# Kernel tuning notes

Measured on AMD Instinct MI355X. Metric: run time of the kernel, lower is better.

Reference implementation:

```python
import jax, jax.numpy as jnp
import numpy as np

B, S, D_IN = 16, 512, 768
HID, OUT = 64, 12
NEG = 1e12


def setup_inputs() -> dict:
    key = jax.random.key(0)
    k1, k2, k3 = jax.random.split(key, 3)
    x = jax.random.normal(k1, (B, S, D_IN), dtype=jnp.float32)
    mask = jnp.ones((B, S), dtype=jnp.float32)
    W = jax.random.normal(k2, (D_IN, HID * OUT * 2), dtype=jnp.float32) * 0.02
    b = jax.random.normal(k3, (HID * OUT * 2,), dtype=jnp.float32) * 0.02
    return {"x": x, "mask": mask, "W": W, "b": b}


def reference(x, mask, W, b):
    Bb, Ss, _ = x.shape
    h, out = HID, OUT
    # QKV-style projection, split into `out` heads of 2h each
    proj = (x @ W + b).reshape(Bb, Ss, out, 2 * h)  # [b, s, out, 2h]
    qw, kw = proj[..., :h], proj[..., h:]           # [b, s, out, h]

    # Sinusoidal position embedding (merge='zero'): interleaved sin/cos
    pos_ids = jnp.arange(Ss, dtype=x.dtype)
    inv_freq = jnp.power(10000.0, -2.0 * jnp.arange(h // 2, dtype=x.dtype) / h)
    ang = pos_ids[:, None] * inv_freq               # [s, h/2]
    sin, cos = jnp.sin(ang), jnp.cos(ang)
    # torch: pos[..., None, 1::2].repeat(1,1,1,2) -> TILED (not interleaved)
    cos_pos = jnp.concatenate([cos, cos], axis=-1)[None, :, None, :]  # [1, s, 1, h]
    sin_pos = jnp.concatenate([sin, sin], axis=-1)[None, :, None, :]

    def rope(w):
        # stack([-w_odd, w_even], -1).reshape -> interleaved rotation partner
        w2 = jnp.stack([-w[..., 1::2], w[..., ::2]], axis=-1).reshape(w.shape)
        return w * cos_pos + w2 * sin_pos

    qw = rope(qw)
    kw = rope(kw)

    logits = jnp.einsum('bmhd,bnhd->bhmn', qw, kw)  # [b, out, s, s]

    pad = mask[:, None, None, :]                    # broadcast over [b, out, s, s]
    logits = logits * pad - (1.0 - pad) * NEG

    tril = jnp.tril(jnp.ones((Ss, Ss), dtype=logits.dtype), -1)
    logits = logits - tril * NEG

    return logits / (h ** 0.5)
```

## Files before the change

kernel.cpp:

```cpp
#include <hip/hip_runtime.h>
#include <stdint.h>

#define DIN   768
#define NPROJ 1536
#define SEQ   512
#define NHEAD 12
#define NBATCH 16
#define NEGV  1000000000000.0f

typedef short bf16x8 __attribute__((ext_vector_type(8)));
typedef float f32x4  __attribute__((ext_vector_type(4)));
typedef unsigned short u16x8 __attribute__((ext_vector_type(8)));

__device__ __forceinline__ unsigned short f2bf(float f) {
    union { float f; unsigned int u; } v; v.f = f;
    return (unsigned short)((v.u + 0x7FFFu + ((v.u >> 16) & 1u)) >> 16);
}
__device__ __forceinline__ float bf2f(unsigned short u) {
    union { unsigned int u; float f; } v; v.u = ((unsigned int)u) << 16;
    return v.f;
}

__device__ __forceinline__ void gl_lds16(const unsigned short* g, unsigned short* l) {
    __builtin_amdgcn_global_load_lds(
        (const __attribute__((address_space(1))) unsigned int*)(uintptr_t)g,
        (__attribute__((address_space(3))) unsigned int*)(uintptr_t)l,
        16, 0, 0);
}

__device__ __forceinline__ void stage128x64(const unsigned short* __restrict__ g,
                                            int gstride, unsigned short* lds,
                                            int w, int lane) {
#pragma unroll
    for (int t = 0; t < 4; t++) {
        int lr = w * 32 + t * 8 + (lane >> 3);
        int c16 = (lane & 7) ^ (lr & 7);
        gl_lds16(g + (size_t)lr * gstride + c16 * 8,
                 lds + (w * 32 + t * 8) * 64);
    }
}
__device__ __forceinline__ int swz(int row, int cg) {
    return row * 64 + ((cg ^ (row & 7)) << 3);
}

__global__ __launch_bounds__(256) void k_prep(const float* __restrict__ X,
                                              unsigned short* __restrict__ Xb,
                                              const float* __restrict__ W,
                                              unsigned short* __restrict__ Wt,
                                              float* __restrict__ trig) {
    __shared__ unsigned short T[64][72];
    const int bid = blockIdx.x, tid = threadIdx.x;
    if (bid < 288) {
        int n0 = (bid % 24) * 64, k0 = (bid / 24) * 64;
#pragma unroll
        for (int it = 0; it < 4; it++) {
            int c = tid + it * 256;
            int kl = c >> 4, nl = (c & 15) * 4;
            float4 v = *(const float4*)&W[(size_t)(k0 + kl) * NPROJ + n0 + nl];
            T[nl + 0][kl] = f2bf(v.x);
            T[nl + 1][kl] = f2bf(v.y);
            T[nl + 2][kl] = f2bf(v.z);
            T[nl + 3][kl] = f2bf(v.w);
        }
        __syncthreads();
#pragma unroll
        for (int it = 0; it < 2; it++) {
            int c = tid + it * 256;
            int nl = c >> 3, kb = (c & 7) * 8;
            *(int4*)&Wt[(size_t)(n0 + nl) * DIN + k0 + kb] = *(int4*)&T[nl][kb];
        }
        return;
    }
    if (bid < 352) {
        int gi = (bid - 288) * 256 + tid;
        int ss = gi >> 5, j = gi & 31;
        const float C = 0.41524101186092034f;
        float cs, sn;
        sincosf((float)ss * exp2f(-(float)j * C), &sn, &cs);
        trig[2 * gi]     = cs;
        trig[2 * gi + 1] = sn;
        return;
    }
    int i = ((bid - 352) * 256 + tid) * 4;
    float4 v = *(const float4*)&X[i];
    short4 s;
    s.x = (short)f2bf(v.x); s.y = (short)f2bf(v.y);
    s.z = (short)f2bf(v.z); s.w = (short)f2bf(v.w);
    *(short4*)&Xb[i] = s;
}

template <bool PRE>
__global__ __launch_bounds__(256) void k_gemm(const float* __restrict__ X,
                                              const unsigned short* __restrict__ Xb,
                                              const unsigned short* __restrict__ Wt,
                                              const float* __restrict__ bias,
                                              const float* __restrict__ trig,
                                              unsigned short* __restrict__ P) {
    __shared__ unsigned short smem[17408];
    unsigned short* sA = smem;
    unsigned short* sB = smem + 8192;
    const int tid = threadIdx.x;
    const int bid = blockIdx.x;
    const int xcd = bid & 7, t0 = bid >> 3;
    const int m0 = (xcd + 8 * (t0 / 12)) * 128;
    const int n0 = (t0 % 12) * 128;
    const int lane = tid & 63, w = tid >> 6;
    const int q = lane >> 4, r = lane & 15;
    const int wm = w >> 1, wn = w & 1;
    f32x4 acc[4][4];
#pragma unroll
    for (int i = 0; i < 4; i++)
#pragma unroll
        for (int j = 0; j < 4; j++) acc[i][j] = (f32x4){0.f, 0.f, 0.f, 0.f};

    const unsigned short* Ag = Xb + (size_t)m0 * DIN;
    const unsigned short* Bg = Wt + (size_t)n0 * DIN;

    for (int k0 = 0; k0 < DIN; k0 += 64) {
        __syncthreads();
        if (PRE) {
            stage128x64(Ag + k0, DIN, sA, w, lane);
        } else {
#pragma unroll
            for (int it = 0; it < 4; it++) {
                int c = tid + it * 256;
                int row = c >> 3, c16 = c & 7;
                const float* xp = &X[(size_t)(m0 + row) * DIN + k0 + c16 * 8];
                float4 v0 = *(const float4*)xp;
                float4 v1 = *(const float4*)(xp + 4);
                u16x8 sv;
                sv[0] = f2bf(v0.x); sv[1] = f2bf(v0.y);
                sv[2] = f2bf(v0.z); sv[3] = f2bf(v0.w);
                sv[4] = f2bf(v1.x); sv[5] = f2bf(v1.y);
                sv[6] = f2bf(v1.z); sv[7] = f2bf(v1.w);
                *(u16x8*)&sA[swz(row, c16)] = sv;
            }
        }
        stage128x64(Bg + k0, DIN, sB, w, lane);
        __syncthreads();
#pragma unroll
        for (int kk = 0; kk < 64; kk += 32) {
            const int cg = (kk >> 3) + q;
            bf16x8 af[4], bfr[4];
#pragma unroll
            for (int t = 0; t < 4; t++)
                af[t] = *(const bf16x8*)&sA[swz(wm * 64 + t * 16 + r, cg)];
#pragma unroll
            for (int t = 0; t < 4; t++)
                bfr[t] = *(const bf16x8*)&sB[swz(wn * 64 + t * 16 + r, cg)];
#pragma unroll
            for (int tm = 0; tm < 4; tm++)
#pragma unroll
                for (int tn = 0; tn < 4; tn++)
                    acc[tm][tn] = __builtin_amdgcn_mfma_f32_16x16x32_bf16(
                        af[tm], bfr[tn], acc[tm][tn], 0, 0, 0);
        }
    }
    float bb[4];
#pragma unroll
    for (int tn = 0; tn < 4; tn++) bb[tn] = bias[n0 + wn * 64 + tn * 16 + r];
    __syncthreads();
    unsigned short* sT = smem;
#pragma unroll
    for (int tm = 0; tm < 4; tm++) {
        int rowb = wm * 64 + tm * 16 + q * 4;
#pragma unroll
        for (int tn = 0; tn < 4; tn++) {
            int col = wn * 64 + tn * 16 + r;
#pragma unroll
            for (int i = 0; i < 4; i++)
                sT[(rowb + i) * 136 + col] = f2bf(acc[tm][tn][i] + bb[tn]);
        }
    }
    __syncthreads();
#pragma unroll
    for (int it = 0; it < 8; it++) {
        int c = tid + it * 256;
        int row = c >> 4, colb = (c & 15) * 8;
        int m = m0 + row;
        int s = m & (SEQ - 1);
        int base = colb & 31;
        union { int4 v; unsigned short u[8]; } pk;
        pk.v = *(int4*)&sT[row * 136 + colb];
        float wv[8];
#pragma unroll
        for (int j = 0; j < 8; j++) wv[j] = bf2f(pk.u[j]);
        const float* tp = &trig[2 * (s * 32 + base)];
#pragma unroll
        for (int p = 0; p < 4; p++) {
            float4 tt = *(const float4*)&tp[4 * p];
            float oe = wv[2 * p] * tt.x - wv[2 * p + 1] * tt.y;
            float oo = wv[2 * p + 1] * tt.z + wv[2 * p] * tt.w;
            pk.u[2 * p]     = f2bf(oe);
            pk.u[2 * p + 1] = f2bf(oo);
        }
        *(int4*)&P[(size_t)m * NPROJ + n0 + colb] = pk.v;
    }
}

__global__ __launch_bounds__(256, 2) void k_attn(const unsigned short* __restrict__ P,
                                                 const float* __restrict__ mask,
                                                 float* __restrict__ out) {
    __shared__ __attribute__((aligned(16))) unsigned short smem[32768];
    const int tid = threadIdx.x;
    const int bi = blockIdx.x;
    const int g  = bi >> 4, rb = bi & 15;
    const int b  = g / NHEAD, h = g % NHEAD;
    const int lane = tid & 63, wn = tid >> 6;
    const int q = lane >> 4, r = lane & 15;
    const int w = wn;
    const size_t obase = ((size_t)((b * NHEAD + h) * SEQ)) * SEQ;
    const int m0 = rb * 32;

    const unsigned short* Pk = P + (size_t)b * SEQ * NPROJ + h * 128 + 64;
#pragma unroll
    for (int c = 0; c < 4; c++)
        if ((c + 1) * 128 > m0)
            stage128x64(Pk + (size_t)(c * 128) * NPROJ, NPROJ,
                        smem + c * 128 * 64, w, lane);

    const unsigned short* Pq = P + (size_t)b * SEQ * NPROJ + h * 128;
    bf16x8 qf[2][2];
#pragma unroll
    for (int rt = 0; rt < 2; rt++)
#pragma unroll
        for (int x2 = 0; x2 < 2; x2++)
            qf[rt][x2] = *(const bf16x8*)
                &Pq[(size_t)(m0 + rt * 16 + r) * NPROJ + x2 * 32 + q * 8];

    f32x4 mk4[8];
#pragma unroll
    for (int t = 0; t < 8; t++)
        mk4[t] = *(const f32x4*)&mask[b * SEQ + (wn * 8 + t) * 16 + q * 4];

    f32x4 acc[8][2];
#pragma unroll
    for (int t = 0; t < 8; t++) {
        acc[t][0] = (f32x4){0.f, 0.f, 0.f, 0.f};
        acc[t][1] = (f32x4){0.f, 0.f, 0.f, 0.f};
    }

    __syncthreads();

#pragma unroll
    for (int t = 0; t < 8; t++) {
        const int ct = wn * 8 + t;
        if (ct >= 2 * rb) {
            bf16x8 kf[2];
#pragma unroll
            for (int x2 = 0; x2 < 2; x2++)
                kf[x2] = *(const bf16x8*)&smem[swz(ct * 16 + r, x2 * 4 + q)];
#pragma unroll
            for (int x2 = 0; x2 < 2; x2++) {
                acc[t][0] = __builtin_amdgcn_mfma_f32_16x16x32_bf16(
                    kf[x2], qf[0][x2], acc[t][0], 0, 0, 0);
                acc[t][1] = __builtin_amdgcn_mfma_f32_16x16x32_bf16(
                    kf[x2], qf[1][x2], acc[t][1], 0, 0, 0);
            }
        }
    }
    __syncthreads();

    float* sOut = (float*)smem;
#pragma unroll
    for (int rt = 0; rt < 2; rt++) {
        const int m = m0 + rt * 16 + r;
#pragma unroll
        for (int t = 0; t < 8; t++) {
            const int ct = wn * 8 + t;
            const int nb = ct * 16 + q * 4;
            f32x4 o;
            if (ct >= 2 * rb) {
#pragma unroll
                for (int j = 0; j < 4; j++)
                    o[j] = (acc[t][rt][j] * mk4[t][j]
                            - (1.f - mk4[t][j]) * NEGV
                            - ((nb + j) < m ? NEGV : 0.f)) * 0.125f;
            } else {
#pragma unroll
                for (int j = 0; j < 4; j++)
                    o[j] = (-(1.f - mk4[t][j]) * NEGV - NEGV) * 0.125f;
            }
            *(f32x4*)&sOut[(rt * 16 + r) * 512 + nb] = o;
        }
    }
    __syncthreads();
    float* od = out + obase + (size_t)m0 * SEQ;
#pragma unroll
    for (int it = 0; it < 16; it++) {
        const int c = tid + it * 256;
        f32x4 v = *(const f32x4*)&sOut[c * 4];
        *(f32x4*)&od[c * 4] = v;
    }
}

extern "C" void kernel_launch(void* const* d_in, const int* in_sizes, int n_in,
                              void* d_out, int out_size, void* d_ws, size_t ws_size,
                              hipStream_t stream) {
    const float* x    = (const float*)d_in[0];
    const float* mask = (const float*)d_in[1];
    const float* W    = (const float*)d_in[2];
    const float* bias = (const float*)d_in[3];
    float* out = (float*)d_out;

    const size_t wtN   = (size_t)NPROJ * DIN;
    const size_t pN    = (size_t)NBATCH * SEQ * NPROJ;
    const size_t xN    = (size_t)NBATCH * SEQ * DIN;
    const size_t trigN = (size_t)SEQ * 32 * 2;
    unsigned short* Wt = (unsigned short*)d_ws;
    unsigned short* P  = Wt + wtN;
    float* trig        = (float*)(P + pN);
    unsigned short* Xb = (unsigned short*)(trig + trigN);
    const bool pre = ws_size >= (wtN + pN + xN) * sizeof(unsigned short)
                               + trigN * sizeof(float);

    const int xblocks = (int)(xN / 1024);
    k_prep<<<pre ? (352 + xblocks) : 352, 256, 0, stream>>>(x, Xb, W, Wt, trig);
    if (pre) {
        k_gemm<true><<<dim3(768), 256, 0, stream>>>(x, Xb, Wt, bias, trig, P);
    } else {
        k_gemm<false><<<dim3(768), 256, 0, stream>>>(x, nullptr, Wt, bias, trig, P);
    }
    k_attn<<<dim3(NBATCH * NHEAD * (SEQ / 32)), 256, 0, stream>>>(P, mask, out);
}
```

Measured before the change: 281.7 us.

## Double-buffer GEMM K-loop LDS tiles to overlap loads with MFMA

Restructures the projection GEMM main loop to use two LDS buffers, issuing global-to-LDS staging of the next K tile before computing on the current one. There is now one barrier per iteration instead of two. The aim is to hide global load latency behind MFMA work. LDS use per block rises from about 34KB to 64KB, which may reduce occupancy. In the non-PRE path the fp32 cast loads sit synchronously in registers before compute, so they overlap less.

New measurement: 276.5 us. No clear change (-1.8%).

```diff
diff --git a/kernel.cpp b/kernel.cpp
--- a/kernel.cpp
+++ b/kernel.cpp
@@ -41,6 +41,25 @@
 }
 __device__ __forceinline__ int swz(int row, int cg) {
     return row * 64 + ((cg ^ (row & 7)) << 3);
+}
+
+__device__ __forceinline__ void stageA_cast(const float* __restrict__ X,
+                                            int m0, int k0,
+                                            unsigned short* buf, int tid) {
+#pragma unroll
+    for (int it = 0; it < 4; it++) {
+        int c = tid + it * 256;
+        int row = c >> 3, c16 = c & 7;
+        const float* xp = &X[(size_t)(m0 + row) * DIN + k0 + c16 * 8];
+        float4 v0 = *(const float4*)xp;
+        float4 v1 = *(const float4*)(xp + 4);
+        u16x8 sv;
+        sv[0] = f2bf(v0.x); sv[1] = f2bf(v0.y);
+        sv[2] = f2bf(v0.z); sv[3] = f2bf(v0.w);
+        sv[4] = f2bf(v1.x); sv[5] = f2bf(v1.y);
+        sv[6] = f2bf(v1.z); sv[7] = f2bf(v1.w);
+        *(u16x8*)&buf[swz(row, c16)] = sv;
+    }
 }
 
 __global__ __launch_bounds__(256) void k_prep(const float* __restrict__ X,
@@ -96,9 +115,7 @@
                                               const float* __restrict__ bias,
                                               const float* __restrict__ trig,
                                               unsigned short* __restrict__ P) {
-    __shared__ unsigned short smem[17408];
-    unsigned short* sA = smem;
-    unsigned short* sB = smem + 8192;
+    __shared__ unsigned short smem[32768];
     const int tid = threadIdx.x;
     const int bid = blockIdx.x;
     const int xcd = bid & 7, t0 = bid >> 3;
@@ -116,38 +133,31 @@
     const unsigned short* Ag = Xb + (size_t)m0 * DIN;
     const unsigned short* Bg = Wt + (size_t)n0 * DIN;
 
-    for (int k0 = 0; k0 < DIN; k0 += 64) {
-        __syncthreads();
-        if (PRE) {
-            stage128x64(Ag + k0, DIN, sA, w, lane);
-        } else {
-#pragma unroll
-            for (int it = 0; it < 4; it++) {
-                int c = tid + it * 256;
-                int row = c >> 3, c16 = c & 7;
-                const float* xp = &X[(size_t)(m0 + row) * DIN + k0 + c16 * 8];
-                float4 v0 = *(const float4*)xp;
-                float4 v1 = *(const float4*)(xp + 4);
-                u16x8 sv;
-                sv[0] = f2bf(v0.x); sv[1] = f2bf(v0.y);
-                sv[2] = f2bf(v0.z); sv[3] = f2bf(v0.w);
-                sv[4] = f2bf(v1.x); sv[5] = f2bf(v1.y);
-                sv[6] = f2bf(v1.z); sv[7] = f2bf(v1.w);
-                *(u16x8*)&sA[swz(row, c16)] = sv;
-            }
-        }
-        stage128x64(Bg + k0, DIN, sB, w, lane);
-        __syncthreads();
+    if (PRE) stage128x64(Ag, DIN, smem, w, lane);
+    else     stageA_cast(X, m0, 0, smem, tid);
+    stage128x64(Bg, DIN, smem + 8192, w, lane);
+    __syncthreads();
+
+    for (int it = 0; it < 12; ++it) {
+        const int c = it & 1;
+        unsigned short* sAc = smem + c * 16384;
+        unsigned short* sBc = sAc + 8192;
+        if (it + 1 < 12) {
+            unsigned short* nxt = smem + (c ^ 1) * 16384;
+            if (PRE) stage128x64(Ag + (it + 1) * 64, DIN, nxt, w, lane);
+            else     stageA_cast(X, m0, (it + 1) * 64, nxt, tid);
+            stage128x64(Bg + (it + 1) * 64, DIN, nxt + 8192, w, lane);
+        }
 #pragma unroll
         for (int kk = 0; kk < 64; kk += 32) {
             const int cg = (kk >> 3) + q;
             bf16x8 af[4], bfr[4];
 #pragma unroll
             for (int t = 0; t < 4; t++)
-                af[t] = *(const bf16x8*)&sA[swz(wm * 64 + t * 16 + r, cg)];
+                af[t] = *(const bf16x8*)&sAc[swz(wm * 64 + t * 16 + r, cg)];
 #pragma unroll
             for (int t = 0; t < 4; t++)
-                bfr[t] = *(const bf16x8*)&sB[swz(wn * 64 + t * 16 + r, cg)];
+                bfr[t] = *(const bf16x8*)&sBc[swz(wn * 64 + t * 16 + r, cg)];
 #pragma unroll
             for (int tm = 0; tm < 4; tm++)
 #pragma unroll
@@ -155,11 +165,11 @@
                     acc[tm][tn] = __builtin_amdgcn_mfma_f32_16x16x32_bf16(
                         af[tm], bfr[tn], acc[tm][tn], 0, 0, 0);
         }
+        __syncthreads();
     }
     float bb[4];
 #pragma unroll
     for (int tn = 0; tn < 4; tn++) bb[tn] = bias[n0 + wn * 64 + tn * 16 + r];
-    __syncthreads();
     unsigned short* sT = smem;
 #pragma unroll
     for (int tm = 0; tm < 4; tm++) {
```
